# Kernel tuning notes

Measured on AMD Instinct MI355X. Metric: run time of the kernel, lower is better.

## Reference

```python
import jax, jax.numpy as jnp
import numpy as np

N_NODES = 50000
N_EDGES = 1600000
EMB_DIM = 128
N_PATH = 2
N_LAYERS = 2
N_HEADS = 8
HEAD_DIM = EMB_DIM // N_HEADS


def setup_inputs() -> dict:
    key = jax.random.key(0)
    ks = jax.random.split(key, 6)
    fs = jax.random.normal(ks[0], (N_PATH, N_NODES, EMB_DIM), dtype=jnp.float32)
    W = jax.random.normal(ks[1], (N_PATH, N_LAYERS, EMB_DIM, EMB_DIM), dtype=jnp.float32) * (1.0 / np.sqrt(EMB_DIM))
    attn_l = jax.random.normal(ks[2], (N_PATH, N_LAYERS, N_HEADS, HEAD_DIM), dtype=jnp.float32) * 0.1
    attn_r = jax.random.normal(ks[3], (N_PATH, N_LAYERS, N_HEADS, HEAD_DIM), dtype=jnp.float32) * 0.1
    bias = jnp.zeros((N_PATH, N_LAYERS, EMB_DIM), dtype=jnp.float32)
    edges = jax.random.randint(ks[4], (N_PATH, 2, N_EDGES), 0, N_NODES, dtype=jnp.int32)
    return {"fs": fs, "W": W, "attn_l": attn_l, "attn_r": attn_r, "bias": bias, "edges": edges}


def gat_conv(h, src, dst, W, al, ar, b):
    # h: [N, F_in]; DGL GATConv, eval mode (dropout off), residual Identity, bias, ELU.
    N = h.shape[0]
    H, D = al.shape
    feat = (h @ W).reshape(N, H, D)                      # fc projection
    el = jnp.einsum('nhd,hd->nh', feat, al)              # [N, H]
    er = jnp.einsum('nhd,hd->nh', feat, ar)              # [N, H]
    e = jax.nn.leaky_relu(el[src] + er[dst], 0.2)        # [E, H]
    # edge softmax over incoming edges of each destination node
    emax = jax.ops.segment_max(e, dst, num_segments=N)   # [N, H], -inf for 0-in-degree
    emax = jnp.where(jnp.isfinite(emax), emax, 0.0)
    ex = jnp.exp(e - emax[dst])                          # [E, H]
    esum = jax.ops.segment_sum(ex, dst, num_segments=N)  # [N, H]
    alpha = ex / jnp.maximum(esum[dst], 1e-9)            # [E, H]
    msg = alpha[:, :, None] * feat[src]                  # [E, H, D]
    rst = jax.ops.segment_sum(msg, dst, num_segments=N)  # [N, H, D]
    rst = rst + h.reshape(N, H, D) + b.reshape(1, H, D)  # residual (Identity) + bias
    out = jax.nn.elu(rst)
    return out.reshape(N, H * D), alpha


def reference(fs, W, attn_l, attn_r, bias, edges):
    semantic_embeddings = []
    element_weights = []
    for p in range(N_PATH):
        h = fs[p]
        src, dst = edges[p, 0], edges[p, 1]
        attn = None
        for l in range(N_LAYERS):
            h, attn = gat_conv(h, src, dst, W[p, l], attn_l[p, l], attn_r[p, l], bias[p, l])
        semantic_embeddings.append(h)
        element_weights.append(attn)
    return jnp.stack(semantic_embeddings), jnp.stack(element_weights)
```

## Files before the change

### kernel.cpp

```cpp
#include <hip/hip_runtime.h>
#include <hip/hip_bf16.h>

#define NND 50000
#define NE  1600000
#define EMB 128
#define NH  8
#define HD  16
#define NB  98

typedef __attribute__((ext_vector_type(8))) short short8v;
typedef __attribute__((ext_vector_type(4))) float f32x4;

__device__ __forceinline__ float lrelu(float x) { return x > 0.f ? x : 0.2f * x; }
__device__ __forceinline__ float elu(float x)   { return x > 0.f ? x : expm1f(x); }

__device__ __forceinline__ unsigned short f2bf(float x) {
    __hip_bfloat16 b = __float2bfloat16(x);
    return *reinterpret_cast<unsigned short*>(&b);
}
__device__ __forceinline__ float bf2f(unsigned short u) {
    __hip_bfloat16 b = *reinterpret_cast<__hip_bfloat16*>(&u);
    return __bfloat162float(b);
}

__global__ __launch_bounds__(256) void hsplit(
    const float* __restrict__ hin, unsigned short* __restrict__ hhi, unsigned short* __restrict__ hlo)
{
    int idx = blockIdx.x * 256 + threadIdx.x;
    const float4* h4 = reinterpret_cast<const float4*>(hin);
    float4 v0 = h4[(size_t)idx * 2];
    float4 v1 = h4[(size_t)idx * 2 + 1];
    float xs[8] = { v0.x, v0.y, v0.z, v0.w, v1.x, v1.y, v1.z, v1.w };
    unsigned short hi[8], lo[8];
    #pragma unroll
    for (int j = 0; j < 8; ++j) {
        hi[j] = f2bf(xs[j]);
        lo[j] = f2bf(xs[j] - bf2f(hi[j]));
    }
    *reinterpret_cast<uint4*>(hhi + (size_t)idx * 8) = *reinterpret_cast<uint4*>(hi);
    *reinterpret_cast<uint4*>(hlo + (size_t)idx * 8) = *reinterpret_cast<uint4*>(lo);
}

__global__ __launch_bounds__(256) void wpack(
    const float* __restrict__ Wm, unsigned short* __restrict__ bphi, unsigned short* __restrict__ bplo)
{
    int s = blockIdx.x * 256 + threadIdx.x;
    if (s >= 2048) return;
    int n    = s >> 8;
    int kt   = (s >> 6) & 3;
    int lane = s & 63;
    int col  = n * 16 + (lane & 15);
    int krow = kt * 32 + ((lane >> 4) << 3);
    #pragma unroll
    for (int j = 0; j < 8; ++j) {
        float x = Wm[(size_t)(krow + j) * EMB + col];
        unsigned short hi = f2bf(x);
        unsigned short lo = f2bf(x - bf2f(hi));
        bphi[(size_t)s * 8 + j] = hi;
        bplo[(size_t)s * 8 + j] = lo;
    }
}

__global__ __launch_bounds__(256) void mfma_gemm(
    const unsigned short* __restrict__ hhi, const unsigned short* __restrict__ hlo,
    const unsigned short* __restrict__ bphi, const unsigned short* __restrict__ bplo,
    const float* __restrict__ alv, const float* __restrict__ arv,
    unsigned short* __restrict__ feat_bf, float* __restrict__ el, float* __restrict__ er)
{
    const int lane = threadIdx.x & 63;
    const int wave = threadIdx.x >> 6;
    const int rowbase = blockIdx.x * 16;

    f32x4 acc[2];
    acc[0] = (f32x4){0.f, 0.f, 0.f, 0.f};
    acc[1] = (f32x4){0.f, 0.f, 0.f, 0.f};

    const int ar  = rowbase + (lane & 15);
    const int car = ar < NND ? ar : NND - 1;
    const int kofs = (lane >> 4) * 8;

    #pragma unroll
    for (int kt = 0; kt < 4; ++kt) {
        const int k0 = kt * 32 + kofs;
        short8v ah = *reinterpret_cast<const short8v*>(hhi + (size_t)car * EMB + k0);
        short8v av = *reinterpret_cast<const short8v*>(hlo + (size_t)car * EMB + k0);
        #pragma unroll
        for (int q = 0; q < 2; ++q) {
            const int nn = wave * 2 + q;
            const size_t bofs = ((size_t)(nn * 4 + kt) * 64 + lane) * 8;
            short8v bh = *reinterpret_cast<const short8v*>(bphi + bofs);
            short8v bl = *reinterpret_cast<const short8v*>(bplo + bofs);
            acc[q] = __builtin_amdgcn_mfma_f32_16x16x32_bf16(ah, bh, acc[q], 0, 0, 0);
            acc[q] = __builtin_amdgcn_mfma_f32_16x16x32_bf16(av, bh, acc[q], 0, 0, 0);
            acc[q] = __builtin_amdgcn_mfma_f32_16x16x32_bf16(ah, bl, acc[q], 0, 0, 0);
        }
    }

    const int colr = lane & 15;
    const int rgrp = lane >> 4;
    const int row0 = rowbase + rgrp * 4;
    #pragma unroll
    for (int q = 0; q < 2; ++q) {
        const int nn = wave * 2 + q;
        f32x4 a = acc[q];
        #pragma unroll
        for (int r = 0; r < 4; ++r) {
            if (row0 + r < NND)
                feat_bf[(size_t)(row0 + r) * EMB + nn * 16 + colr] = f2bf(a[r]);
        }
        const float alc = alv[nn * 16 + colr];
        const float arc = arv[nn * 16 + colr];
        float pl[4], pr[4];
        #pragma unroll
        for (int r = 0; r < 4; ++r) { pl[r] = a[r] * alc; pr[r] = a[r] * arc; }
        #pragma unroll
        for (int mask = 1; mask < 16; mask <<= 1) {
            #pragma unroll
            for (int r = 0; r < 4; ++r) {
                pl[r] += __shfl_xor(pl[r], mask);
                pr[r] += __shfl_xor(pr[r], mask);
            }
        }
        if (colr == 0) {
            #pragma unroll
            for (int r = 0; r < 4; ++r) {
                int row = row0 + r;
                if (row < NND) {
                    el[row * NH + nn] = pl[r];
                    er[row * NH + nn] = pr[r];
                }
            }
        }
    }
}

__global__ __launch_bounds__(256) void bucket_count(
    const int* __restrict__ dst, int* __restrict__ bcnt)
{
    __shared__ int hist[NB];
    const int t = threadIdx.x;
    for (int b = t; b < NB; b += 256) hist[b] = 0;
    __syncthreads();
    const int e0 = blockIdx.x * 2048 + t * 8;
    #pragma unroll
    for (int j = 0; j < 8; ++j) {
        int e = e0 + j;
        if (e < NE) atomicAdd(&hist[dst[e] >> 9], 1);
    }
    __syncthreads();
    for (int b = t; b < NB; b += 256)
        if (hist[b]) atomicAdd(&bcnt[b], hist[b]);
}

__global__ __launch_bounds__(128) void scan_bucket(
    const int* __restrict__ bcnt, int* __restrict__ bbase, int* __restrict__ bcur)
{
    __shared__ int s[128];
    const int t = threadIdx.x;
    s[t] = (t < NB) ? bcnt[t] : 0;
    __syncthreads();
    for (int off = 1; off < 128; off <<= 1) {
        int v = (t >= off) ? s[t - off] : 0;
        __syncthreads();
        s[t] += v;
        __syncthreads();
    }
    int excl = (t > 0) ? s[t - 1] : 0;
    if (t <= NB) bbase[t] = excl;
    if (t < NB)  bcur[t]  = excl;
}

__global__ __launch_bounds__(256) void bucket_scatter(
    const int* __restrict__ src, const int* __restrict__ dst,
    int* __restrict__ bcur, int2* __restrict__ ebuf)
{
    __shared__ int hist[NB];
    __shared__ int base[NB];
    __shared__ int lcur[NB];
    const int t  = threadIdx.x;
    const int e0 = blockIdx.x * 2048 + t * 8;

    for (int b = t; b < NB; b += 256) { hist[b] = 0; lcur[b] = 0; }
    __syncthreads();

    int sj[8], dj[8];
    bool vj[8];
    #pragma unroll
    for (int j = 0; j < 8; ++j) {
        int e = e0 + j;
        vj[j] = (e < NE);
        if (vj[j]) {
            sj[j] = src[e];
            dj[j] = dst[e];
            atomicAdd(&hist[dj[j] >> 9], 1);
        }
    }
    __syncthreads();
    for (int b = t; b < NB; b += 256) {
        int c = hist[b];
        base[b] = c > 0 ? atomicAdd(&bcur[b], c) : 0;
    }
    __syncthreads();
    #pragma unroll
    for (int j = 0; j < 8; ++j) {
        if (vj[j]) {
            int b   = dj[j] >> 9;
            int off = atomicAdd(&lcur[b], 1);
            ebuf[(size_t)base[b] + off] = make_int2(sj[j], dj[j]);
        }
    }
}

__global__ __launch_bounds__(1024) void bucket_fill(
    const int* __restrict__ bbase, const int2* __restrict__ ebuf,
    int* __restrict__ rowptr, int* __restrict__ csrsrc)
{
    __shared__ int hist[512];
    __shared__ int excl[512];
    const int b    = blockIdx.x;
    const int n0   = b << 9;
    const int t    = threadIdx.x;
    const int base = bbase[b];
    const int cnt  = bbase[b + 1] - base;

    if (t < 512) hist[t] = 0;
    __syncthreads();
    for (int i = t; i < cnt; i += 1024)
        atomicAdd(&hist[ebuf[base + i].y - n0], 1);
    __syncthreads();
    if (t < 512) excl[t] = hist[t];
    __syncthreads();
    for (int off = 1; off < 512; off <<= 1) {
        int v = 0;
        if (t < 512 && t >= off) v = excl[t - off];
        __syncthreads();
        if (t < 512) excl[t] += v;
        __syncthreads();
    }
    if (t < 512) {
        int e = excl[t] - hist[t];
        int n = n0 + t;
        if (n < NND) rowptr[n] = base + e;
        hist[t] = e;
    }
    if (b == NB - 1 && t == 0) rowptr[NND] = NE;
    __syncthreads();
    for (int i = t; i < cnt; i += 1024) {
        int2 ed = ebuf[base + i];
        int p = atomicAdd(&hist[ed.y - n0], 1);
        csrsrc[base + p] = ed.x;
    }
}

__global__ __launch_bounds__(256) void gather_agg(
    const int* __restrict__ rowptr, const int* __restrict__ csrsrc,
    const float* __restrict__ el, const float* __restrict__ er,
    const unsigned int* __restrict__ featu,
    const float* __restrict__ hin_f32,
    const unsigned int* __restrict__ hin_hi,
    const unsigned int* __restrict__ hin_lo,
    const float* __restrict__ bias,
    float* __restrict__ esum_out,
    float* __restrict__ hout_f32,
    unsigned int* __restrict__ hhi_out,
    unsigned int* __restrict__ hlo_out)
{
    const int wid  = (blockIdx.x * blockDim.x + threadIdx.x) >> 6;
    const int lane = threadIdx.x & 63;
    if (wid >= NND) return;
    const int n  = wid;
    const int h  = lane >> 3;
    const int j8 = lane & 7;

    const float ern = er[n * NH + h];
    const int r0 = __builtin_amdgcn_readfirstlane(rowptr[n]);
    const int r1 = __builtin_amdgcn_readfirstlane(rowptr[n + 1]);

    float acc0 = 0.f, acc1 = 0.f, es = 0.f;

    const int nfull = r0 + ((r1 - r0) & ~7);
    int i = r0;
    for (; i < nfull; i += 8) {
        int   sv = csrsrc[i + j8];
        float w  = expf(lrelu(el[sv * NH + h] + ern));
        int sjs[8];
        #pragma unroll
        for (int j = 0; j < 8; ++j) sjs[j] = __shfl(sv, j);
        unsigned int vs[8];
        #pragma unroll
        for (int j = 0; j < 8; ++j) vs[j] = featu[(size_t)sjs[j] * 64 + lane];
        #pragma unroll
        for (int j = 0; j < 8; ++j) {
            float wj = __shfl(w, (lane & 56) | j);
            es  += wj;
            acc0 = fmaf(wj, __uint_as_float(vs[j] << 16), acc0);
            acc1 = fmaf(wj, __uint_as_float(vs[j] & 0xffff0000u), acc1);
        }
    }
    if (i < r1) {
        const int m = r1 - i;
        int idx = i + j8;
        int sv  = csrsrc[idx < r1 ? idx : (r1 - 1)];
        float w = 0.f;
        if (j8 < m) w = expf(lrelu(el[sv * NH + h] + ern));
        #pragma unroll
        for (int j = 0; j < 8; ++j) {
            if (j >= m) break;
            int   sj = __shfl(sv, j);
            float wj = __shfl(w, (lane & 56) | j);
            unsigned int v = featu[(size_t)sj * 64 + lane];
            es  += wj;
            acc0 = fmaf(wj, __uint_as_float(v << 16), acc0);
            acc1 = fmaf(wj, __uint_as_float(v & 0xffff0000u), acc1);
        }
    }

    if (j8 == 0) esum_out[n * NH + h] = es;
    const float inv = 1.f / fmaxf(es, 1e-9f);

    float h0, h1;
    if (hin_f32) {
        float2 hv = reinterpret_cast<const float2*>(hin_f32)[(size_t)n * 64 + lane];
        h0 = hv.x; h1 = hv.y;
    } else {
        unsigned int hiu = hin_hi[(size_t)n * 64 + lane];
        unsigned int lou = hin_lo[(size_t)n * 64 + lane];
        h0 = __uint_as_float(hiu << 16) + __uint_as_float(lou << 16);
        h1 = __uint_as_float(hiu & 0xffff0000u) + __uint_as_float(lou & 0xffff0000u);
    }
    float o0 = elu(fmaf(acc0, inv, h0 + bias[lane * 2]));
    float o1 = elu(fmaf(acc1, inv, h1 + bias[lane * 2 + 1]));

    if (hout_f32) {
        reinterpret_cast<float2*>(hout_f32)[(size_t)n * 64 + lane] = make_float2(o0, o1);
    } else {
        unsigned short hi0 = f2bf(o0), hi1 = f2bf(o1);
        unsigned short lo0 = f2bf(o0 - bf2f(hi0)), lo1 = f2bf(o1 - bf2f(hi1));
        hhi_out[(size_t)n * 64 + lane] = (unsigned int)hi0 | ((unsigned int)hi1 << 16);
        hlo_out[(size_t)n * 64 + lane] = (unsigned int)lo0 | ((unsigned int)lo1 << 16);
    }
}

__global__ __launch_bounds__(256) void alpha_write(
    const int* __restrict__ src, const int* __restrict__ dst,
    const float* __restrict__ el, const float* __restrict__ er,
    const float* __restrict__ esum, float* __restrict__ aout)
{
    int tid = blockIdx.x * blockDim.x + threadIdx.x;
    if (tid >= NE * NH) return;
    int e = tid >> 3;
    int h = tid & 7;
    int s = src[e], d = dst[e];
    float x = lrelu(el[s * NH + h] + er[d * NH + h]);
    float a = expf(x) / fmaxf(esum[d * NH + h], 1e-9f);
    aout[(size_t)e * NH + h] = a;
}

extern "C" void kernel_launch(void* const* d_in, const int* in_sizes, int n_in,
                              void* d_out, int out_size, void* d_ws, size_t ws_size,
                              hipStream_t stream) {
    const float* fs   = (const float*)d_in[0];
    const float* W    = (const float*)d_in[1];
    const float* al   = (const float*)d_in[2];
    const float* ar   = (const float*)d_in[3];
    const float* bias = (const float*)d_in[4];
    const int*   edges= (const int*)d_in[5];

    float* out       = (float*)d_out;
    float* out_emb   = out;
    float* out_alpha = out + (size_t)2 * NND * EMB;

    char* ws = (char*)d_ws;
    unsigned short* feat_bf = (unsigned short*)ws; ws += (size_t)NND * EMB * 2;
    unsigned short* hhi     = (unsigned short*)ws; ws += (size_t)NND * EMB * 2;
    unsigned short* hlo     = (unsigned short*)ws; ws += (size_t)NND * EMB * 2;
    float*          el      = (float*)ws;          ws += (size_t)NND * NH * 4;
    float*          er      = (float*)ws;          ws += (size_t)NND * NH * 4;
    float*          esum    = (float*)ws;          ws += (size_t)NND * NH * 4;
    int*            rowptr  = (int*)ws;            ws += (size_t)(NND + 1) * 4;
    int*            bcnt    = (int*)ws;            ws += (size_t)128 * 4;
    int*            bbase   = (int*)ws;            ws += (size_t)132 * 4;
    int*            bcur    = (int*)ws;            ws += (size_t)128 * 4;
    int*            csrsrc  = (int*)ws;            ws += (size_t)NE * 4;
    int2*           ebuf    = (int2*)ws;           ws += (size_t)NE * 8;
    unsigned short* bphi    = (unsigned short*)ws; ws += (size_t)16384 * 2;
    unsigned short* bplo    = (unsigned short*)ws; ws += (size_t)16384 * 2;

    unsigned int* featu = (unsigned int*)feat_bf;
    unsigned int* hhi_u = (unsigned int*)hhi;
    unsigned int* hlo_u = (unsigned int*)hlo;

    for (int p = 0; p < 2; ++p) {
        const int* src = edges + (size_t)p * 2 * NE;
        const int* dst = src + NE;

        hipMemsetAsync(bcnt, 0, (size_t)128 * 4, stream);
        bucket_count<<<(NE + 2047) / 2048, 256, 0, stream>>>(dst, bcnt);
        scan_bucket<<<1, 128, 0, stream>>>(bcnt, bbase, bcur);
        bucket_scatter<<<(NE + 2047) / 2048, 256, 0, stream>>>(src, dst, bcur, ebuf);
        bucket_fill<<<NB, 1024, 0, stream>>>(bbase, ebuf, rowptr, csrsrc);

        for (int l = 0; l < 2; ++l) {
            const float* fsp  = fs + (size_t)p * NND * EMB;
            const float* Wl   = W    + (size_t)(p * 2 + l) * EMB * EMB;
            const float* alv  = al   + (size_t)(p * 2 + l) * NH * HD;
            const float* arv  = ar   + (size_t)(p * 2 + l) * NH * HD;
            const float* bl   = bias + (size_t)(p * 2 + l) * EMB;

            wpack<<<8, 256, 0, stream>>>(Wl, bphi, bplo);
            if (l == 0)
                hsplit<<<NND * EMB / 8 / 256, 256, 0, stream>>>(fsp, hhi, hlo);

            mfma_gemm<<<(NND + 15) / 16, 256, 0, stream>>>(hhi, hlo, bphi, bplo, alv, arv, feat_bf, el, er);

            if (l == 0) {
                gather_agg<<<(NND + 3) / 4, 256, 0, stream>>>(
                    rowptr, csrsrc, el, er, featu,
                    fsp, nullptr, nullptr, bl, esum,
                    nullptr, hhi_u, hlo_u);
            } else {
                gather_agg<<<(NND + 3) / 4, 256, 0, stream>>>(
                    rowptr, csrsrc, el, er, featu,
                    nullptr, hhi_u, hlo_u, bl, esum,
                    out_emb + (size_t)p * NND * EMB, nullptr, nullptr);
                alpha_write<<<((size_t)NE * NH + 255) / 256, 256, 0, stream>>>(
                    src, dst, el, er, esum, out_alpha + (size_t)p * NE * NH);
            }
        }
    }
}
```

Measured before the change: 690.4 us.

## Pack bucket edges into one int and batch 16-edge gathers in aggregation

Edges in the bucket buffer are packed into a single 32-bit word (src shifted left 9 bits, local dst in the low bits), halving the scratch traffic of the CSR build. The aggregation kernel now loads source indices directly per lane (broadcast loads) instead of shuffling, issues 16 feature gathers at once to raise memory-level parallelism, and computes edge weights redundantly per lane rather than sharing them through shuffles. expf is replaced by __expf in aggregation and alpha writing, which trades a little accuracy for cheaper exponentials. More registers are used per thread for the 16-wide batch.

```diff
diff --git a/kernel.cpp b/kernel.cpp
--- a/kernel.cpp
+++ b/kernel.cpp
@@ -172,7 +172,7 @@
 
 __global__ __launch_bounds__(256) void bucket_scatter(
     const int* __restrict__ src, const int* __restrict__ dst,
-    int* __restrict__ bcur, int2* __restrict__ ebuf)
+    int* __restrict__ bcur, int* __restrict__ ebuf)
 {
     __shared__ int hist[NB];
     __shared__ int base[NB];
@@ -206,13 +206,13 @@
         if (vj[j]) {
             int b   = dj[j] >> 9;
             int off = atomicAdd(&lcur[b], 1);
-            ebuf[(size_t)base[b] + off] = make_int2(sj[j], dj[j]);
+            ebuf[(size_t)base[b] + off] = (sj[j] << 9) | (dj[j] & 511);
         }
     }
 }
 
 __global__ __launch_bounds__(1024) void bucket_fill(
-    const int* __restrict__ bbase, const int2* __restrict__ ebuf,
+    const int* __restrict__ bbase, const int* __restrict__ ebuf,
     int* __restrict__ rowptr, int* __restrict__ csrsrc)
 {
     __shared__ int hist[512];
@@ -226,7 +226,7 @@
     if (t < 512) hist[t] = 0;
     __syncthreads();
     for (int i = t; i < cnt; i += 1024)
-        atomicAdd(&hist[ebuf[base + i].y - n0], 1);
+        atomicAdd(&hist[ebuf[base + i] & 511], 1);
     __syncthreads();
     if (t < 512) excl[t] = hist[t];
     __syncthreads();
@@ -246,9 +246,9 @@
     if (b == NB - 1 && t == 0) rowptr[NND] = NE;
     __syncthreads();
     for (int i = t; i < cnt; i += 1024) {
-        int2 ed = ebuf[base + i];
-        int p = atomicAdd(&hist[ed.y - n0], 1);
-        csrsrc[base + p] = ed.x;
+        int ed = ebuf[base + i];
+        int p = atomicAdd(&hist[ed & 511], 1);
+        csrsrc[base + p] = ed >> 9;
     }
 }
 
@@ -268,9 +268,8 @@
     const int wid  = (blockIdx.x * blockDim.x + threadIdx.x) >> 6;
     const int lane = threadIdx.x & 63;
     if (wid >= NND) return;
-    const int n  = wid;
-    const int h  = lane >> 3;
-    const int j8 = lane & 7;
+    const int n = wid;
+    const int h = lane >> 3;
 
     const float ern = er[n * NH + h];
     const int r0 = __builtin_amdgcn_readfirstlane(rowptr[n]);
@@ -278,44 +277,50 @@
 
     float acc0 = 0.f, acc1 = 0.f, es = 0.f;
 
-    const int nfull = r0 + ((r1 - r0) & ~7);
     int i = r0;
-    for (; i < nfull; i += 8) {
-        int   sv = csrsrc[i + j8];
-        float w  = expf(lrelu(el[sv * NH + h] + ern));
-        int sjs[8];
-        #pragma unroll
-        for (int j = 0; j < 8; ++j) sjs[j] = __shfl(sv, j);
+    for (; i + 16 <= r1; i += 16) {
+        int sj[16];
+        #pragma unroll
+        for (int j = 0; j < 16; ++j) sj[j] = csrsrc[i + j];
+        unsigned int vs[16];
+        #pragma unroll
+        for (int j = 0; j < 16; ++j) vs[j] = featu[(size_t)sj[j] * 64 + lane];
+        float w[16];
+        #pragma unroll
+        for (int j = 0; j < 16; ++j) w[j] = __expf(lrelu(el[sj[j] * NH + h] + ern));
+        #pragma unroll
+        for (int j = 0; j < 16; ++j) {
+            es  += w[j];
+            acc0 = fmaf(w[j], __uint_as_float(vs[j] << 16), acc0);
+            acc1 = fmaf(w[j], __uint_as_float(vs[j] & 0xffff0000u), acc1);
+        }
+    }
+    if (i + 8 <= r1) {
+        int sj[8];
+        #pragma unroll
+        for (int j = 0; j < 8; ++j) sj[j] = csrsrc[i + j];
         unsigned int vs[8];
         #pragma unroll
-        for (int j = 0; j < 8; ++j) vs[j] = featu[(size_t)sjs[j] * 64 + lane];
+        for (int j = 0; j < 8; ++j) vs[j] = featu[(size_t)sj[j] * 64 + lane];
         #pragma unroll
         for (int j = 0; j < 8; ++j) {
-            float wj = __shfl(w, (lane & 56) | j);
-            es  += wj;
-            acc0 = fmaf(wj, __uint_as_float(vs[j] << 16), acc0);
-            acc1 = fmaf(wj, __uint_as_float(vs[j] & 0xffff0000u), acc1);
-        }
-    }
-    if (i < r1) {
-        const int m = r1 - i;
-        int idx = i + j8;
-        int sv  = csrsrc[idx < r1 ? idx : (r1 - 1)];
-        float w = 0.f;
-        if (j8 < m) w = expf(lrelu(el[sv * NH + h] + ern));
-        #pragma unroll
-        for (int j = 0; j < 8; ++j) {
-            if (j >= m) break;
-            int   sj = __shfl(sv, j);
-            float wj = __shfl(w, (lane & 56) | j);
-            unsigned int v = featu[(size_t)sj * 64 + lane];
-            es  += wj;
-            acc0 = fmaf(wj, __uint_as_float(v << 16), acc0);
-            acc1 = fmaf(wj, __uint_as_float(v & 0xffff0000u), acc1);
-        }
-    }
-
-    if (j8 == 0) esum_out[n * NH + h] = es;
+            float w = __expf(lrelu(el[sj[j] * NH + h] + ern));
+            es  += w;
+            acc0 = fmaf(w, __uint_as_float(vs[j] << 16), acc0);
+            acc1 = fmaf(w, __uint_as_float(vs[j] & 0xffff0000u), acc1);
+        }
+        i += 8;
+    }
+    for (; i < r1; ++i) {
+        int sj = csrsrc[i];
+        unsigned int v = featu[(size_t)sj * 64 + lane];
+        float w = __expf(lrelu(el[sj * NH + h] + ern));
+        es  += w;
+        acc0 = fmaf(w, __uint_as_float(v << 16), acc0);
+        acc1 = fmaf(w, __uint_as_float(v & 0xffff0000u), acc1);
+    }
+
+    if ((lane & 7) == 0) esum_out[n * NH + h] = es;
     const float inv = 1.f / fmaxf(es, 1e-9f);
 
     float h0, h1;
@@ -352,7 +357,7 @@
     int h = tid & 7;
     int s = src[e], d = dst[e];
     float x = lrelu(el[s * NH + h] + er[d * NH + h]);
-    float a = expf(x) / fmaxf(esum[d * NH + h], 1e-9f);
+    float a = __expf(x) / fmaxf(esum[d * NH + h], 1e-9f);
     aout[(size_t)e * NH + h] = a;
 }
 
@@ -382,7 +387,7 @@
     int*            bbase   = (int*)ws;            ws += (size_t)132 * 4;
     int*            bcur    = (int*)ws;            ws += (size_t)128 * 4;
     int*            csrsrc  = (int*)ws;            ws += (size_t)NE * 4;
-    int2*           ebuf    = (int2*)ws;           ws += (size_t)NE * 8;
+    int*            ebuf    = (int*)ws;            ws += (size_t)NE * 4;
     unsigned short* bphi    = (unsigned short*)ws; ws += (size_t)16384 * 2;
     unsigned short* bplo    = (unsigned short*)ws; ws += (size_t)16384 * 2;
 
```

New measurement: 667.0 us. 3.4% less time.
